# Optimization experiments

Measured on AMD Instinct MI355X. Metric: run time of the kernel, lower is better.

The kernel has to match this reference:

```python
import jax, jax.numpy as jnp
import numpy as np

N, H, E, D, L = 100000, 20000, 1600000, 64, 3
F = 4 * D  # ffn hidden = out_dim * 4


def _ln(x, g, b, eps=1e-5):
    mu = x.mean(-1, keepdims=True)
    var = ((x - mu) ** 2).mean(-1, keepdims=True)
    return (x - mu) * jax.lax.rsqrt(var + eps) * g + b


def _gconv(x, W, b, src, dst, inv_sqrt_src, inv_sqrt_dst, n_dst):
    # DGL GraphConv, norm='both': D_dst^{-1/2} A D_src^{-1/2} (x W) + b
    h = (x * inv_sqrt_src[:, None]) @ W
    agg = jax.ops.segment_sum(h[src], dst, num_segments=n_dst)
    return agg * inv_sqrt_dst[:, None] + b


def setup_inputs() -> dict:
    key = jax.random.key(0)
    ks = jax.random.split(key, 24)
    s = 0.05
    inp = {
        'node_features': jax.random.normal(ks[0], (N, D), jnp.float32),
        'edge_src': jax.random.randint(ks[1], (E,), 0, N),
        'edge_dst': jax.random.randint(ks[2], (E,), 0, H),
        'n_hyper': H,
        # stacked per-layer params [L, ...]
        'Wn2h': jax.random.normal(ks[3], (L, D, D), jnp.float32) * s,
        'bn2h': jnp.zeros((L, D), jnp.float32),
        'Wh2n': jax.random.normal(ks[4], (L, D, D), jnp.float32) * s,
        'bh2n': jnp.zeros((L, D), jnp.float32),
        'W1': jax.random.normal(ks[5], (L, D, F), jnp.float32) * s,
        'b1': jnp.zeros((L, F), jnp.float32),
        'W2': jax.random.normal(ks[6], (L, F, D), jnp.float32) * s,
        'b2': jnp.zeros((L, D), jnp.float32),
        'g1': jnp.ones((L, D), jnp.float32),
        'be1': jnp.zeros((L, D), jnp.float32),
        'g2': jnp.ones((L, D), jnp.float32),
        'be2': jnp.zeros((L, D), jnp.float32),
        'gF': jnp.ones((D,), jnp.float32),
        'bF': jnp.zeros((D,), jnp.float32),
        'Wo': jax.random.normal(ks[7], (D, D), jnp.float32) * s,
        'bo': jnp.zeros((D,), jnp.float32),
    }
    return inp


def reference(node_features, edge_src, edge_dst, n_hyper, Wn2h, bn2h, Wh2n, bh2n,
              W1, b1, W2, b2, g1, be1, g2, be2, gF, bF, Wo, bo):
    n_nodes = node_features.shape[0]
    ones = jnp.ones(edge_src.shape[0], node_features.dtype)
    deg_node = jnp.clip(jax.ops.segment_sum(ones, edge_src, num_segments=n_nodes), 1.0)
    deg_hyp = jnp.clip(jax.ops.segment_sum(ones, edge_dst, num_segments=n_hyper), 1.0)
    is_node = jax.lax.rsqrt(deg_node)  # node out-degree^{-1/2}
    is_hyp = jax.lax.rsqrt(deg_hyp)    # hyperedge in-degree^{-1/2}

    def step(h, p):
        Wa, ba, Wb, bb, w1, c1, w2, c2, gg1, ee1, gg2, ee2 = p
        # node -> hyperedge conv (unused attention output is overwritten in the original)
        h_hyper = _gconv(h, Wa, ba, edge_src, edge_dst, is_node, is_hyp, n_hyper)
        # hyperedge -> node conv on reversed graph (degrees swap roles)
        h_node = _gconv(h_hyper, Wb, bb, edge_dst, edge_src, is_hyp, is_node, n_nodes)
        h = _ln(h + h_node, gg1, ee1)
        h_ffn = jax.nn.relu(h @ w1 + c1) @ w2 + c2
        h = _ln(h + h_ffn, gg2, ee2)
        return h, None

    h, _ = jax.lax.scan(step, node_features,
                        (Wn2h, bn2h, Wh2n, bh2n, W1, b1, W2, b2, g1, be1, g2, be2))
    h = _ln(h, gF, bF)
    return h @ Wo + bo
```

## Files before the change

### kernel.cpp

```cpp
#include <hip/hip_runtime.h>

#define HYP 20000
#define NLAYER 3
#define NB_H 313
#define NB_N 391
#define PT 4096

typedef __attribute__((ext_vector_type(8))) short short8;
typedef __attribute__((ext_vector_type(4))) float floatx4;

static __device__ __forceinline__ unsigned short f2bf(float f){
  union { float f; unsigned u; } v; v.f = f;
  unsigned r = v.u + 0x7FFF + ((v.u >> 16) & 1);
  return (unsigned short)(r >> 16);
}

__global__ __launch_bounds__(256) void k_hist(const int* __restrict__ src,
    const int* __restrict__ dst, int E, int* __restrict__ bh, int* __restrict__ bn){
  __shared__ int lh[NB_H + NB_N];
  int tid = threadIdx.x;
  for (int i = tid; i < NB_H + NB_N; i += 256) lh[i] = 0;
  __syncthreads();
  for (int i = blockIdx.x*256 + tid; i < E; i += gridDim.x*256){
    atomicAdd(&lh[dst[i] >> 6], 1);
    atomicAdd(&lh[NB_H + (src[i] >> 8)], 1);
  }
  __syncthreads();
  for (int i = tid; i < NB_H; i += 256) if (lh[i]) atomicAdd(&bh[i], lh[i]);
  for (int i = tid; i < NB_N; i += 256) if (lh[NB_H+i]) atomicAdd(&bn[i], lh[NB_H+i]);
}

__global__ __launch_bounds__(256) void k_bscan(const int* __restrict__ bh,
    const int* __restrict__ bn, int* __restrict__ bstart_h, int* __restrict__ gcur_h,
    int* __restrict__ bstart_n, int* __restrict__ gcur_n){
  __shared__ int ssc[4];
  __shared__ int scarry;
  int tid = threadIdx.x, lane = tid & 63, wv = tid >> 6;
  if (tid == 0) scarry = 0;
  __syncthreads();
  for (int base = 0; base < NB_H; base += 256){
    int i = base + tid; int v = (i < NB_H) ? bh[i] : 0; int x = v;
    #pragma unroll
    for (int o = 1; o < 64; o <<= 1){ int t = __shfl_up(x,o,64); if (lane >= o) x += t; }
    if (lane == 63) ssc[wv] = x;
    __syncthreads();
    int add = (wv>0?ssc[0]:0)+(wv>1?ssc[1]:0)+(wv>2?ssc[2]:0);
    int c = scarry;
    if (i < NB_H){ int ex = c + add + x - v; bstart_h[i] = ex; gcur_h[i] = ex; }
    __syncthreads();
    if (tid == 255) scarry = c + ssc[0]+ssc[1]+ssc[2]+ssc[3];
    __syncthreads();
  }
  if (tid == 0){ bstart_h[NB_H] = scarry; scarry = 0; }
  __syncthreads();
  for (int base = 0; base < NB_N; base += 256){
    int i = base + tid; int v = (i < NB_N) ? bn[i] : 0; int x = v;
    #pragma unroll
    for (int o = 1; o < 64; o <<= 1){ int t = __shfl_up(x,o,64); if (lane >= o) x += t; }
    if (lane == 63) ssc[wv] = x;
    __syncthreads();
    int add = (wv>0?ssc[0]:0)+(wv>1?ssc[1]:0)+(wv>2?ssc[2]:0);
    int c = scarry;
    if (i < NB_N){ int ex = c + add + x - v; bstart_n[i] = ex; gcur_n[i] = ex; }
    __syncthreads();
    if (tid == 255) scarry = c + ssc[0]+ssc[1]+ssc[2]+ssc[3];
    __syncthreads();
  }
  if (tid == 0) bstart_n[NB_N] = scarry;
}

__global__ __launch_bounds__(256) void k_partition(const int* __restrict__ keys,
    const int* __restrict__ pays, int E, int keyshift, int nb,
    int* __restrict__ gcur, unsigned* __restrict__ Ebuf){
  __shared__ unsigned sst[PT];
  __shared__ int lh[NB_N], lpre[NB_N], gb[NB_N];
  __shared__ int ssc[4];
  __shared__ int scarry;
  int tid = threadIdx.x, lane = tid & 63, wv = tid >> 6;
  int base = blockIdx.x*PT;
  int m = min(PT, E - base);
  for (int i = tid; i < nb; i += 256) lh[i] = 0;
  if (tid == 0) scarry = 0;
  __syncthreads();
  unsigned en[16]; int rk[16];
  #pragma unroll
  for (int j = 0; j < 16; ++j){
    int i = base + j*256 + tid;
    if (i < E){
      unsigned k = (unsigned)keys[i], p = (unsigned)pays[i];
      en[j] = (k << keyshift) | p;
      rk[j] = atomicAdd(&lh[en[j] >> 23], 1);
    } else { en[j] = 0; rk[j] = -1; }
  }
  __syncthreads();
  for (int b2 = 0; b2 < nb; b2 += 256){
    int i = b2 + tid; int v = (i < nb) ? lh[i] : 0; int x = v;
    #pragma unroll
    for (int o = 1; o < 64; o <<= 1){ int t = __shfl_up(x,o,64); if (lane >= o) x += t; }
    if (lane == 63) ssc[wv] = x;
    __syncthreads();
    int add = (wv>0?ssc[0]:0)+(wv>1?ssc[1]:0)+(wv>2?ssc[2]:0);
    int c = scarry;
    if (i < nb) lpre[i] = c + add + x - v;
    __syncthreads();
    if (tid == 255) scarry = c + ssc[0]+ssc[1]+ssc[2]+ssc[3];
    __syncthreads();
  }
  for (int i = tid; i < nb; i += 256) gb[i] = atomicAdd(&gcur[i], lh[i]);
  #pragma unroll
  for (int j = 0; j < 16; ++j){
    if (rk[j] >= 0){
      int bk = en[j] >> 23;
      sst[lpre[bk] + rk[j]] = en[j];
    }
  }
  __syncthreads();
  for (int j = tid; j < m; j += 256){
    unsigned e = sst[j];
    int bk = e >> 23;
    Ebuf[gb[bk] + (j - lpre[bk])] = e;
  }
}

__global__ __launch_bounds__(256) void k_build(const unsigned* __restrict__ Ebuf,
    const int* __restrict__ bstart, int keyshift, int ipb, int paymask, int limit,
    int* __restrict__ off, float* __restrict__ isv, int* __restrict__ csr){
  __shared__ int lcnt[256], lpre2[256], lcur[256];
  int tid = threadIdx.x, lane = tid & 63, wv = tid >> 6;
  int b = blockIdx.x;
  int base = bstart[b], m = bstart[b+1] - base;
  for (int i = tid; i < ipb; i += 256) lcnt[i] = 0;
  __syncthreads();
  for (int i = tid; i < m; i += 256){
    unsigned e = Ebuf[base + i];
    atomicAdd(&lcnt[(e >> keyshift) & (ipb-1)], 1);
  }
  __syncthreads();
  if (wv == 0){
    int carry = 0;
    for (int c = 0; c < ipb; c += 64){
      int li = c + lane;
      int v = lcnt[li]; int x = v;
      #pragma unroll
      for (int o = 1; o < 64; o <<= 1){ int t = __shfl_up(x,o,64); if (lane >= o) x += t; }
      int ex = carry + x - v;
      int id = b*ipb + li;
      if (id <= limit) off[id] = base + ex;
      if (id < limit) isv[id] = rsqrtf((float)(v > 0 ? v : 1));
      lpre2[li] = ex;
      carry += __shfl(x, 63, 64);
    }
  }
  for (int i = tid; i < ipb; i += 256) lcur[i] = 0;
  __syncthreads();
  for (int i = tid; i < m; i += 256){
    unsigned e = Ebuf[base + i];
    int li = (e >> keyshift) & (ipb-1);
    int pos = base + lpre2[li] + atomicAdd(&lcur[li], 1);
    csr[pos] = (int)(e & (unsigned)paymask);
  }
}

__global__ void k_prescale(const float* __restrict__ x, const float* __restrict__ isn,
                           unsigned short* __restrict__ xb, int nrows){
  int i = blockIdx.x*blockDim.x + threadIdx.x;
  int st = gridDim.x*blockDim.x;
  int tot = nrows*64;
  for (; i < tot; i += st){ xb[i] = f2bf(x[i]*isn[i >> 6]); }
}

__global__ void k_cvtall(const float* __restrict__ W1, const float* __restrict__ W2,
                         const float* __restrict__ Wa, const float* __restrict__ Wb,
                         const float* __restrict__ Wo,
                         unsigned short* __restrict__ W1T, unsigned short* __restrict__ W2T,
                         unsigned short* __restrict__ WaT, unsigned short* __restrict__ WbT,
                         unsigned short* __restrict__ WoT){
  int st = gridDim.x*blockDim.x;
  int t0 = blockIdx.x*blockDim.x + threadIdx.x;
  for (int j = t0; j < NLAYER*16384; j += st){
    int l = j >> 14, n = (j >> 6) & 255, k = j & 63;
    W1T[j] = f2bf(W1[l*16384 + k*256 + n]);
  }
  for (int j = t0; j < NLAYER*16384; j += st){
    int l = j >> 14, o = (j >> 8) & 63, kk = j & 255;
    W2T[j] = f2bf(W2[l*16384 + kk*64 + o]);
  }
  for (int j = t0; j < NLAYER*4096; j += st){
    int l = j >> 12, n = (j >> 6) & 63, k = j & 63;
    WaT[j] = f2bf(Wa[l*4096 + k*64 + n]);
  }
  for (int j = t0; j < NLAYER*4096; j += st){
    int l = j >> 12, n = (j >> 6) & 63, k = j & 63;
    WbT[j] = f2bf(Wb[l*4096 + k*64 + n]);
  }
  for (int j = t0; j < 4096; j += st){
    int n = (j >> 6) & 63, k = j & 63;
    WoT[j] = f2bf(Wo[k*64 + n]);
  }
}

template<int LSTR>
static __device__ __forceinline__ void stage64(const unsigned short* __restrict__ gsrc,
    unsigned short* __restrict__ ldst, int tid, int rows){
  int nch = rows*8;
  for (int idx = tid; idx < nch; idx += 256){
    int row = idx >> 3, kc = (idx & 7)*8;
    uint4 v = *(const uint4*)&gsrc[row*64 + kc];
    *(uint4*)&ldst[row*LSTR + kc] = v;
  }
}

#define ACC8(u) \
  a0 += __uint_as_float(u.x << 16); a1 += __uint_as_float(u.x & 0xFFFF0000u); \
  a2 += __uint_as_float(u.y << 16); a3 += __uint_as_float(u.y & 0xFFFF0000u); \
  a4 += __uint_as_float(u.z << 16); a5 += __uint_as_float(u.z & 0xFFFF0000u); \
  a6 += __uint_as_float(u.w << 16); a7 += __uint_as_float(u.w & 0xFFFF0000u);

__global__ __launch_bounds__(256) void k_gather8(const unsigned short* __restrict__ feat,
    const int* __restrict__ csr, const int* __restrict__ off,
    unsigned short* __restrict__ agg, int nrows){
  int lane = threadIdx.x & 63, wvi = threadIdx.x >> 6;
  int g = lane >> 3;
  int ch = (lane & 7) * 8;
  int r = blockIdx.x*4 + wvi, stride = gridDim.x*4;
  for (; r < nrows; r += stride){
    int b = off[r], e = off[r+1];
    float a0=0,a1=0,a2=0,a3=0,a4=0,a5=0,a6=0,a7=0;
    int t = b;
    for (; t + 32 <= e; t += 32){
      int s0 = csr[t + g];
      int s1 = csr[t + 8 + g];
      int s2 = csr[t + 16 + g];
      int s3 = csr[t + 24 + g];
      uint4 u0 = *(const uint4*)&feat[(size_t)s0*64 + ch];
      uint4 u1 = *(const uint4*)&feat[(size_t)s1*64 + ch];
      uint4 u2 = *(const uint4*)&feat[(size_t)s2*64 + ch];
      uint4 u3 = *(const uint4*)&feat[(size_t)s3*64 + ch];
      ACC8(u0); ACC8(u1); ACC8(u2); ACC8(u3);
    }
    for (; t + 16 <= e; t += 16){
      int s0 = csr[t + g];
      int s1 = csr[t + 8 + g];
      uint4 u0 = *(const uint4*)&feat[(size_t)s0*64 + ch];
      uint4 u1 = *(const uint4*)&feat[(size_t)s1*64 + ch];
      ACC8(u0); ACC8(u1);
    }
    for (; t < e; t += 8){
      int idx = t + g;
      bool valid = idx < e;
      int s = csr[valid ? idx : b];
      uint4 u = *(const uint4*)&feat[(size_t)s*64 + ch];
      if (!valid){ u.x = 0; u.y = 0; u.z = 0; u.w = 0; }
      ACC8(u);
    }
    #pragma unroll
    for (int o = 8; o <= 32; o <<= 1){
      a0 += __shfl_xor(a0,o,64); a1 += __shfl_xor(a1,o,64);
      a2 += __shfl_xor(a2,o,64); a3 += __shfl_xor(a3,o,64);
      a4 += __shfl_xor(a4,o,64); a5 += __shfl_xor(a5,o,64);
      a6 += __shfl_xor(a6,o,64); a7 += __shfl_xor(a7,o,64);
    }
    if (g == 0){
      uint4 w;
      w.x = (unsigned)f2bf(a0) | ((unsigned)f2bf(a1) << 16);
      w.y = (unsigned)f2bf(a2) | ((unsigned)f2bf(a3) << 16);
      w.z = (unsigned)f2bf(a4) | ((unsigned)f2bf(a5) << 16);
      w.w = (unsigned)f2bf(a6) | ((unsigned)f2bf(a7) << 16);
      *(uint4*)&agg[(size_t)r*64 + ch] = w;
    }
  }
}

__global__ __launch_bounds__(256) void k_mmA(const unsigned short* __restrict__ aggb,
    const unsigned short* __restrict__ WaT, const float* __restrict__ bias,
    const float* __restrict__ ihy, unsigned short* __restrict__ ouths, int nrows){
  __shared__ unsigned short sWb[64*72];
  int tid = threadIdx.x;
  int lane = tid & 63, w = tid >> 6;
  int quad = lane >> 4, n16 = lane & 15;
  stage64<72>(WaT, sWb, tid, 64);
  __syncthreads();
  int rowbase = blockIdx.x*64 + w*16;
  int arow = min(rowbase + n16, nrows-1);
  short8 a0 = *(const short8*)&aggb[(size_t)arow*64 + quad*8];
  short8 a1 = *(const short8*)&aggb[(size_t)arow*64 + 32 + quad*8];
  float ih[4];
  #pragma unroll
  for (int r = 0; r < 4; ++r) ih[r] = ihy[min(rowbase + quad*4 + r, nrows-1)];
  #pragma unroll
  for (int ot = 0; ot < 4; ++ot){
    floatx4 c = (floatx4){0.f,0.f,0.f,0.f};
    short8 b0 = *(const short8*)&sWb[(ot*16+n16)*72 + quad*8];
    short8 b1 = *(const short8*)&sWb[(ot*16+n16)*72 + 32 + quad*8];
    c = __builtin_amdgcn_mfma_f32_16x16x32_bf16(a0, b0, c, 0, 0, 0);
    c = __builtin_amdgcn_mfma_f32_16x16x32_bf16(a1, b1, c, 0, 0, 0);
    float bl = bias[ot*16 + n16];
    #pragma unroll
    for (int r = 0; r < 4; ++r){
      int rr = rowbase + quad*4 + r;
      if (rr < nrows)
        ouths[(size_t)rr*64 + ot*16 + n16] = f2bf(fmaf(c[r], ih[r], bl) * ih[r]);
    }
  }
}

__global__ __launch_bounds__(256) void k_fused(
    const unsigned short* __restrict__ aggb,
    const unsigned short* __restrict__ WbT,
    const float* __restrict__ bbg,
    const float* __restrict__ isn,
    const float* __restrict__ hin,
    const float* __restrict__ g1v, const float* __restrict__ be1v,
    const unsigned short* __restrict__ W1T, const float* __restrict__ b1g,
    const unsigned short* __restrict__ W2T, const float* __restrict__ b2g,
    const float* __restrict__ g2v, const float* __restrict__ be2v,
    float* __restrict__ Outp, unsigned short* __restrict__ Qs, int nrows)
{
  __shared__ unsigned short sW1T[128*72];
  __shared__ unsigned short sW2T[64*136];
  __shared__ unsigned short sPH[4*16*72];
  unsigned short* sWb = sW1T;
  int tid = threadIdx.x;
  int lane = tid & 63, w = tid >> 6;
  int quad = lane >> 4, n16 = lane & 15;
  int rb[2];
  rb[0] = blockIdx.x*128 + w*16;
  rb[1] = rb[0] + 64;

  stage64<72>(WbT, sWb, tid, 64);
  __syncthreads();

  float pP[2][4][4];
  float isr[2][4];
  #pragma unroll
  for (int s = 0; s < 2; ++s){
    int arow = min(rb[s] + n16, nrows-1);
    short8 a0 = *(const short8*)&aggb[(size_t)arow*64 + quad*8];
    short8 a1 = *(const short8*)&aggb[(size_t)arow*64 + 32 + quad*8];
    #pragma unroll
    for (int r = 0; r < 4; ++r) isr[s][r] = isn[min(rb[s] + quad*4 + r, nrows-1)];
    #pragma unroll
    for (int ot = 0; ot < 4; ++ot){
      floatx4 c = (floatx4){0.f,0.f,0.f,0.f};
      short8 b0 = *(const short8*)&sWb[(ot*16+n16)*72 + quad*8];
      short8 b1 = *(const short8*)&sWb[(ot*16+n16)*72 + 32 + quad*8];
      c = __builtin_amdgcn_mfma_f32_16x16x32_bf16(a0, b0, c, 0, 0, 0);
      c = __builtin_amdgcn_mfma_f32_16x16x32_bf16(a1, b1, c, 0, 0, 0);
      float bb = bbg[ot*16 + n16];
      #pragma unroll
      for (int r = 0; r < 4; ++r){
        int rr = min(rb[s] + quad*4 + r, nrows-1);
        pP[s][ot][r] = fmaf(c[r], isr[s][r], bb) + hin[(size_t)rr*64 + ot*16 + n16];
      }
    }
  }
  {
    float gl[4], bl[4];
    #pragma unroll
    for (int ot = 0; ot < 4; ++ot){ gl[ot] = g1v[ot*16+n16]; bl[ot] = be1v[ot*16+n16]; }
    #pragma unroll
    for (int s = 0; s < 2; ++s)
      #pragma unroll
      for (int r = 0; r < 4; ++r){
        float sv = (pP[s][0][r] + pP[s][1][r]) + (pP[s][2][r] + pP[s][3][r]);
        float q = fmaf(pP[s][0][r], pP[s][0][r], pP[s][1][r]*pP[s][1][r]) +
                  fmaf(pP[s][2][r], pP[s][2][r], pP[s][3][r]*pP[s][3][r]);
        #pragma unroll
        for (int o = 8; o >= 1; o >>= 1){
          sv += __shfl_xor(sv, o, 64);
          q  += __shfl_xor(q, o, 64);
        }
        float mu = sv*(1.f/64.f);
        float var = fmaf(-mu, mu, q*(1.f/64.f));
        float rs = rsqrtf(var + 1e-5f);
        #pragma unroll
        for (int ot = 0; ot < 4; ++ot)
          pP[s][ot][r] = fmaf((pP[s][ot][r]-mu)*rs, gl[ot], bl[ot]);
      }
  }
  unsigned short* myP = &sPH[w*16*72];
  short8 p0[2], p1[2];
  #pragma unroll
  for (int s = 0; s < 2; ++s){
    #pragma unroll
    for (int ot = 0; ot < 4; ++ot)
      #pragma unroll
      for (int r = 0; r < 4; ++r)
        myP[(quad*4 + r)*72 + ot*16 + n16] = f2bf(pP[s][ot][r]);
    p0[s] = *(const short8*)&myP[n16*72 + quad*8];
    p1[s] = *(const short8*)&myP[n16*72 + 32 + quad*8];
  }

  floatx4 acc2[2][4];
  #pragma unroll
  for (int s = 0; s < 2; ++s)
    #pragma unroll
    for (int t = 0; t < 4; ++t) acc2[s][t] = (floatx4){0.f,0.f,0.f,0.f};
  unsigned short* myHc = &sPH[w*16*72];

  for (int hb = 0; hb < 2; ++hb){
    __syncthreads();
    stage64<72>(W1T + hb*128*64, sW1T, tid, 128);
    for (int idx = tid; idx < 1024; idx += 256){
      int o = idx >> 4, kc = (idx & 15)*8;
      uint4 v = *(const uint4*)&W2T[o*256 + hb*128 + kc];
      *(uint4*)&sW2T[o*136 + kc] = v;
    }
    __syncthreads();

    for (int ck = 0; ck < 4; ++ck){
      #pragma unroll
      for (int s = 0; s < 2; ++s){
        #pragma unroll
        for (int nt = 0; nt < 2; ++nt){
          int nn = ck*32 + nt*16 + n16;
          floatx4 c = (floatx4){0.f,0.f,0.f,0.f};
          short8 b0 = *(const short8*)&sW1T[nn*72 + quad*8];
          short8 b1f = *(const short8*)&sW1T[nn*72 + 32 + quad*8];
          c = __builtin_amdgcn_mfma_f32_16x16x32_bf16(p0[s], b0, c, 0, 0, 0);
          c = __builtin_amdgcn_mfma_f32_16x16x32_bf16(p1[s], b1f, c, 0, 0, 0);
          float bb = b1g[hb*128 + nn];
          #pragma unroll
          for (int r = 0; r < 4; ++r){
            float h = fmaxf(c[r] + bb, 0.f);
            myHc[(quad*4 + r)*40 + nt*16 + n16] = f2bf(h);
          }
        }
        short8 a2 = *(const short8*)&myHc[n16*40 + quad*8];
        #pragma unroll
        for (int ot = 0; ot < 4; ++ot){
          short8 b2f = *(const short8*)&sW2T[(ot*16 + n16)*136 + ck*32 + quad*8];
          acc2[s][ot] = __builtin_amdgcn_mfma_f32_16x16x32_bf16(a2, b2f, acc2[s][ot], 0, 0, 0);
        }
      }
    }
  }

  float gl[4], bel[4];
  #pragma unroll
  for (int ot = 0; ot < 4; ++ot){ gl[ot] = g2v[ot*16 + n16]; bel[ot] = be2v[ot*16 + n16]; }
  #pragma unroll
  for (int s = 0; s < 2; ++s){
    float pre[4][4];
    #pragma unroll
    for (int ot = 0; ot < 4; ++ot){
      float b2c = b2g[ot*16 + n16];
      #pragma unroll
      for (int r = 0; r < 4; ++r)
        pre[ot][r] = acc2[s][ot][r] + b2c + pP[s][ot][r];
    }
    #pragma unroll
    for (int r = 0; r < 4; ++r){
      float sv = (pre[0][r] + pre[1][r]) + (pre[2][r] + pre[3][r]);
      float q = fmaf(pre[0][r], pre[0][r], pre[1][r]*pre[1][r]) +
                fmaf(pre[2][r], pre[2][r], pre[3][r]*pre[3][r]);
      #pragma unroll
      for (int o = 8; o >= 1; o >>= 1){
        sv += __shfl_xor(sv, o, 64);
        q  += __shfl_xor(q, o, 64);
      }
      float mu = sv*(1.f/64.f);
      float var = fmaf(-mu, mu, q*(1.f/64.f));
      float rs = rsqrtf(var + 1e-5f);
      int rr = rb[s] + quad*4 + r;
      if (rr < nrows){
        float isr2 = isn[rr];
        #pragma unroll
        for (int ot = 0; ot < 4; ++ot){
          float ov = fmaf((pre[ot][r]-mu)*rs, gl[ot], bel[ot]);
          Outp[(size_t)rr*64 + ot*16 + n16] = ov;
          Qs[(size_t)rr*64 + ot*16 + n16] = f2bf(ov * isr2);
        }
      }
    }
  }
}

__global__ __launch_bounds__(256) void k_final(const float* __restrict__ Q,
    const unsigned short* __restrict__ WoT, const float* __restrict__ bog,
    const float* __restrict__ gF, const float* __restrict__ bF,
    float* __restrict__ out, int nrows){
  __shared__ unsigned short sWb[64*72];
  int tid = threadIdx.x;
  int lane = tid & 63, w = tid >> 6;
  int quad = lane >> 4, n16 = lane & 15;
  stage64<72>(WoT, sWb, tid, 64);
  __syncthreads();
  int rowbase = blockIdx.x*64 + w*16;
  int arow = min(rowbase + n16, nrows-1);
  float4 q0 = *(const float4*)&Q[(size_t)arow*64 + quad*8];
  float4 q1 = *(const float4*)&Q[(size_t)arow*64 + quad*8 + 4];
  float4 q2 = *(const float4*)&Q[(size_t)arow*64 + 32 + quad*8];
  float4 q3 = *(const float4*)&Q[(size_t)arow*64 + 32 + quad*8 + 4];
  float s = (q0.x+q0.y+q0.z+q0.w) + (q1.x+q1.y+q1.z+q1.w)
          + (q2.x+q2.y+q2.z+q2.w) + (q3.x+q3.y+q3.z+q3.w);
  float qq = (q0.x*q0.x+q0.y*q0.y+q0.z*q0.z+q0.w*q0.w)
           + (q1.x*q1.x+q1.y*q1.y+q1.z*q1.z+q1.w*q1.w)
           + (q2.x*q2.x+q2.y*q2.y+q2.z*q2.z+q2.w*q2.w)
           + (q3.x*q3.x+q3.y*q3.y+q3.z*q3.z+q3.w*q3.w);
  s += __shfl_xor(s, 16, 64);  qq += __shfl_xor(qq, 16, 64);
  s += __shfl_xor(s, 32, 64);  qq += __shfl_xor(qq, 32, 64);
  float mu = s*(1.f/64.f);
  float var = fmaf(-mu, mu, qq*(1.f/64.f));
  float rs = rsqrtf(var + 1e-5f);
  float4 g0 = *(const float4*)&gF[quad*8];
  float4 g1 = *(const float4*)&gF[quad*8 + 4];
  float4 g2 = *(const float4*)&gF[32 + quad*8];
  float4 g3 = *(const float4*)&gF[32 + quad*8 + 4];
  float4 f0 = *(const float4*)&bF[quad*8];
  float4 f1 = *(const float4*)&bF[quad*8 + 4];
  float4 f2 = *(const float4*)&bF[32 + quad*8];
  float4 f3 = *(const float4*)&bF[32 + quad*8 + 4];
  short8 a0, a1;
  a0[0]=f2bf(fmaf((q0.x-mu)*rs, g0.x, f0.x)); a0[1]=f2bf(fmaf((q0.y-mu)*rs, g0.y, f0.y));
  a0[2]=f2bf(fmaf((q0.z-mu)*rs, g0.z, f0.z)); a0[3]=f2bf(fmaf((q0.w-mu)*rs, g0.w, f0.w));
  a0[4]=f2bf(fmaf((q1.x-mu)*rs, g1.x, f1.x)); a0[5]=f2bf(fmaf((q1.y-mu)*rs, g1.y, f1.y));
  a0[6]=f2bf(fmaf((q1.z-mu)*rs, g1.z, f1.z)); a0[7]=f2bf(fmaf((q1.w-mu)*rs, g1.w, f1.w));
  a1[0]=f2bf(fmaf((q2.x-mu)*rs, g2.x, f2.x)); a1[1]=f2bf(fmaf((q2.y-mu)*rs, g2.y, f2.y));
  a1[2]=f2bf(fmaf((q2.z-mu)*rs, g2.z, f2.z)); a1[3]=f2bf(fmaf((q2.w-mu)*rs, g2.w, f2.w));
  a1[4]=f2bf(fmaf((q3.x-mu)*rs, g3.x, f3.x)); a1[5]=f2bf(fmaf((q3.y-mu)*rs, g3.y, f3.y));
  a1[6]=f2bf(fmaf((q3.z-mu)*rs, g3.z, f3.z)); a1[7]=f2bf(fmaf((q3.w-mu)*rs, g3.w, f3.w));
  #pragma unroll
  for (int ot = 0; ot < 4; ++ot){
    floatx4 c = (floatx4){0.f,0.f,0.f,0.f};
    short8 b0 = *(const short8*)&sWb[(ot*16+n16)*72 + quad*8];
    short8 b1 = *(const short8*)&sWb[(ot*16+n16)*72 + 32 + quad*8];
    c = __builtin_amdgcn_mfma_f32_16x16x32_bf16(a0, b0, c, 0, 0, 0);
    c = __builtin_amdgcn_mfma_f32_16x16x32_bf16(a1, b1, c, 0, 0, 0);
    float bol = bog[ot*16 + n16];
    #pragma unroll
    for (int r = 0; r < 4; ++r){
      int rr = rowbase + quad*4 + r;
      if (rr < nrows) out[(size_t)rr*64 + ot*16 + n16] = c[r] + bol;
    }
  }
}

extern "C" void kernel_launch(void* const* d_in, const int* in_sizes, int n_in,
                              void* d_out, int out_size, void* d_ws, size_t ws_size,
                              hipStream_t stream){
  const float* nf   = (const float*)d_in[0];
  const int*   esrc = (const int*)d_in[1];
  const int*   edst = (const int*)d_in[2];
  const float* Wn2h = (const float*)d_in[4];
  const float* bn2h = (const float*)d_in[5];
  const float* Wh2n = (const float*)d_in[6];
  const float* bh2n = (const float*)d_in[7];
  const float* W1   = (const float*)d_in[8];
  const float* b1   = (const float*)d_in[9];
  const float* W2   = (const float*)d_in[10];
  const float* b2   = (const float*)d_in[11];
  const float* g1   = (const float*)d_in[12];
  const float* be1  = (const float*)d_in[13];
  const float* g2   = (const float*)d_in[14];
  const float* be2  = (const float*)d_in[15];
  const float* gF   = (const float*)d_in[16];
  const float* bF   = (const float*)d_in[17];
  const float* Wo   = (const float*)d_in[18];
  const float* bo   = (const float*)d_in[19];
  const int N = in_sizes[0] / 64;
  const int E = in_sizes[1];
  const int H = HYP;
  float* out = (float*)d_out;

  char* w = (char*)d_ws;
  auto carve = [&](size_t bytes) -> char* {
    char* p = w; w += (bytes + 255) & ~(size_t)255; return p;
  };
  int* bh = (int*)carve((size_t)(NB_H + NB_N)*4);
  int* bn = bh + NB_H;
  int* bstart_h = (int*)carve((size_t)(NB_H+1)*4);
  int* gcur_h   = (int*)carve((size_t)NB_H*4);
  int* bstart_n = (int*)carve((size_t)(NB_N+1)*4);
  int* gcur_n   = (int*)carve((size_t)NB_N*4);
  unsigned* Ebuf_h = (unsigned*)carve((size_t)E*4);
  unsigned* Ebuf_n = (unsigned*)carve((size_t)E*4);
  int*   off_h = (int*)carve((size_t)(H+1)*4);
  int*   off_n = (int*)carve((size_t)(N+1)*4);
  float* is_h  = (float*)carve((size_t)H*4);
  float* is_n  = (float*)carve((size_t)N*4);
  int*   csr_h = (int*)carve((size_t)E*4);
  int*   csr_n = (int*)carve((size_t)E*4);
  unsigned short* aggxb = (unsigned short*)carve((size_t)H*64*2);
  unsigned short* agghb = (unsigned short*)carve((size_t)N*64*2);
  float* Qb    = (float*)carve((size_t)N*64*4);
  unsigned short* hhsb = (unsigned short*)carve((size_t)H*64*2);
  unsigned short* xb0  = (unsigned short*)carve((size_t)N*64*2);
  unsigned short* Qs   = (unsigned short*)carve((size_t)N*64*2);
  unsigned short* W1g16 = (unsigned short*)carve((size_t)NLAYER*64*256*2);
  unsigned short* W2g16 = (unsigned short*)carve((size_t)NLAYER*256*64*2);
  unsigned short* Wag16 = (unsigned short*)carve((size_t)NLAYER*4096*2);
  unsigned short* Wbg16 = (unsigned short*)carve((size_t)NLAYER*4096*2);
  unsigned short* Wog16 = (unsigned short*)carve((size_t)4096*2);

  hipMemsetAsync(bh, 0, (size_t)(NB_H + NB_N)*4, stream);
  k_cvtall<<<96, 256, 0, stream>>>(W1, W2, Wn2h, Wh2n, Wo,
                                   W1g16, W2g16, Wag16, Wbg16, Wog16);
  k_hist<<<512, 256, 0, stream>>>(esrc, edst, E, bh, bn);
  k_bscan<<<1, 256, 0, stream>>>(bh, bn, bstart_h, gcur_h, bstart_n, gcur_n);
  k_partition<<<(E + PT - 1)/PT, 256, 0, stream>>>(edst, esrc, E, 17, NB_H, gcur_h, Ebuf_h);
  k_partition<<<(E + PT - 1)/PT, 256, 0, stream>>>(esrc, edst, E, 15, NB_N, gcur_n, Ebuf_n);
  k_build<<<NB_H, 256, 0, stream>>>(Ebuf_h, bstart_h, 17, 64, 0x1FFFF, H, off_h, is_h, csr_h);
  k_build<<<NB_N, 256, 0, stream>>>(Ebuf_n, bstart_n, 15, 256, 0x7FFF, N, off_n, is_n, csr_n);
  k_prescale<<<4096, 256, 0, stream>>>(nf, is_n, xb0, N);

  const int NB64 = (N + 63)/64;
  const int NB128 = (N + 127)/128;
  const int HB64 = (H + 63)/64;
  for (int l = 0; l < NLAYER; ++l){
    const float* hin = (l == 0) ? nf : Qb;
    const unsigned short* hsrc = (l == 0) ? xb0 : Qs;
    k_gather8<<<2048, 256, 0, stream>>>(hsrc, csr_h, off_h, aggxb, H);
    k_mmA<<<HB64, 256, 0, stream>>>(aggxb, Wag16 + l*4096, bn2h + l*64, is_h, hhsb, H);
    k_gather8<<<2048, 256, 0, stream>>>(hhsb, csr_n, off_n, agghb, N);
    k_fused<<<NB128, 256, 0, stream>>>(agghb, Wbg16 + l*4096, bh2n + l*64, is_n, hin,
                                       g1 + l*64, be1 + l*64,
                                       W1g16 + l*64*256, b1 + l*256,
                                       W2g16 + l*256*64, b2 + l*64,
                                       g2 + l*64, be2 + l*64, Qb, Qs, N);
  }
  k_final<<<NB64, 256, 0, stream>>>(Qb, Wog16, bo, gF, bF, out, N);
}
```

Baseline: 537.5 us.

## Restructure fused FFN kernel to 64-row blocks with swizzled LDS weight tiles

The fused node-side kernel now processes 64 rows per block instead of 128, stages W1/W2 in four 64-wide chunks into XOR-swizzled unpadded LDS tiles, and sets an occupancy hint of 6 blocks per SM. This lowers LDS and register use per block so more blocks can be resident and avoids bank conflicts, at the cost of re-staging weights for twice as many blocks and more barriers. The hyperedge matmul kernel moves to 64-thread blocks of 16 rows, and prescale is vectorised to 8 elements per thread.

```diff
diff --git a/kernel.cpp b/kernel.cpp
--- a/kernel.cpp
+++ b/kernel.cpp
@@ -165,8 +165,18 @@
                            unsigned short* __restrict__ xb, int nrows){
   int i = blockIdx.x*blockDim.x + threadIdx.x;
   int st = gridDim.x*blockDim.x;
-  int tot = nrows*64;
-  for (; i < tot; i += st){ xb[i] = f2bf(x[i]*isn[i >> 6]); }
+  int tot = nrows*8;
+  for (; i < tot; i += st){
+    float s = isn[i >> 3];
+    float4 v0 = *(const float4*)&x[(size_t)i*8];
+    float4 v1 = *(const float4*)&x[(size_t)i*8 + 4];
+    uint4 o;
+    o.x = (unsigned)f2bf(v0.x*s) | ((unsigned)f2bf(v0.y*s) << 16);
+    o.y = (unsigned)f2bf(v0.z*s) | ((unsigned)f2bf(v0.w*s) << 16);
+    o.z = (unsigned)f2bf(v1.x*s) | ((unsigned)f2bf(v1.y*s) << 16);
+    o.w = (unsigned)f2bf(v1.z*s) | ((unsigned)f2bf(v1.w*s) << 16);
+    *(uint4*)&xb[(size_t)i*8] = o;
+  }
 }
 
 __global__ void k_cvtall(const float* __restrict__ W1, const float* __restrict__ W2,
@@ -208,6 +218,22 @@
     uint4 v = *(const uint4*)&gsrc[row*64 + kc];
     *(uint4*)&ldst[row*LSTR + kc] = v;
   }
+}
+
+static __device__ __forceinline__ void stage_swz(const unsigned short* __restrict__ g,
+    int gs, unsigned short* __restrict__ l, int tid){
+  #pragma unroll
+  for (int it = 0; it < 2; ++it){
+    int c = it*256 + tid;
+    int row = c >> 3, s = c & 7;
+    uint4 v = *(const uint4*)&g[row*gs + s*8];
+    *(uint4*)&l[(row << 6) + ((((unsigned)(s ^ row)) & 7u) << 3)] = v;
+  }
+}
+
+static __device__ __forceinline__ short8 rdswz(const unsigned short* __restrict__ l,
+    int row, int slot){
+  return *(const short8*)&l[(row << 6) + ((((unsigned)(slot ^ row)) & 7u) << 3)];
 }
 
 #define ACC8(u) \
@@ -271,16 +297,18 @@
   }
 }
 
-__global__ __launch_bounds__(256) void k_mmA(const unsigned short* __restrict__ aggb,
+__global__ __launch_bounds__(64) void k_mmA(const unsigned short* __restrict__ aggb,
     const unsigned short* __restrict__ WaT, const float* __restrict__ bias,
     const float* __restrict__ ihy, unsigned short* __restrict__ ouths, int nrows){
   __shared__ unsigned short sWb[64*72];
-  int tid = threadIdx.x;
-  int lane = tid & 63, w = tid >> 6;
+  int lane = threadIdx.x;
   int quad = lane >> 4, n16 = lane & 15;
-  stage64<72>(WaT, sWb, tid, 64);
-  __syncthreads();
-  int rowbase = blockIdx.x*64 + w*16;
+  for (int idx = lane; idx < 512; idx += 64){
+    int row = idx >> 3, kc = (idx & 7)*8;
+    *(uint4*)&sWb[row*72 + kc] = *(const uint4*)&WaT[row*64 + kc];
+  }
+  __syncthreads();
+  int rowbase = blockIdx.x*16;
   int arow = min(rowbase + n16, nrows-1);
   short8 a0 = *(const short8*)&aggb[(size_t)arow*64 + quad*8];
   short8 a1 = *(const short8*)&aggb[(size_t)arow*64 + 32 + quad*8];
@@ -304,7 +332,7 @@
   }
 }
 
-__global__ __launch_bounds__(256) void k_fused(
+__global__ __launch_bounds__(256, 6) void k_fused(
     const unsigned short* __restrict__ aggb,
     const unsigned short* __restrict__ WbT,
     const float* __restrict__ bbg,
@@ -316,41 +344,37 @@
     const float* __restrict__ g2v, const float* __restrict__ be2v,
     float* __restrict__ Outp, unsigned short* __restrict__ Qs, int nrows)
 {
-  __shared__ unsigned short sW1T[128*72];
-  __shared__ unsigned short sW2T[64*136];
+  __shared__ unsigned short sA[64*64];
+  __shared__ unsigned short sB[64*64];
   __shared__ unsigned short sPH[4*16*72];
-  unsigned short* sWb = sW1T;
   int tid = threadIdx.x;
   int lane = tid & 63, w = tid >> 6;
   int quad = lane >> 4, n16 = lane & 15;
-  int rb[2];
-  rb[0] = blockIdx.x*128 + w*16;
-  rb[1] = rb[0] + 64;
-
-  stage64<72>(WbT, sWb, tid, 64);
-  __syncthreads();
-
-  float pP[2][4][4];
-  float isr[2][4];
-  #pragma unroll
-  for (int s = 0; s < 2; ++s){
-    int arow = min(rb[s] + n16, nrows-1);
+  int rb = blockIdx.x*64 + w*16;
+
+  stage_swz(WbT, 64, sA, tid);
+  __syncthreads();
+
+  float pP[4][4];
+  float isr[4];
+  {
+    int arow = min(rb + n16, nrows-1);
     short8 a0 = *(const short8*)&aggb[(size_t)arow*64 + quad*8];
     short8 a1 = *(const short8*)&aggb[(size_t)arow*64 + 32 + quad*8];
     #pragma unroll
-    for (int r = 0; r < 4; ++r) isr[s][r] = isn[min(rb[s] + quad*4 + r, nrows-1)];
+    for (int r = 0; r < 4; ++r) isr[r] = isn[min(rb + quad*4 + r, nrows-1)];
     #pragma unroll
     for (int ot = 0; ot < 4; ++ot){
       floatx4 c = (floatx4){0.f,0.f,0.f,0.f};
-      short8 b0 = *(const short8*)&sWb[(ot*16+n16)*72 + quad*8];
-      short8 b1 = *(const short8*)&sWb[(ot*16+n16)*72 + 32 + quad*8];
+      short8 b0 = rdswz(sA, ot*16+n16, quad);
+      short8 b1 = rdswz(sA, ot*16+n16, 4+quad);
       c = __builtin_amdgcn_mfma_f32_16x16x32_bf16(a0, b0, c, 0, 0, 0);
       c = __builtin_amdgcn_mfma_f32_16x16x32_bf16(a1, b1, c, 0, 0, 0);
       float bb = bbg[ot*16 + n16];
       #pragma unroll
       for (int r = 0; r < 4; ++r){
-        int rr = min(rb[s] + quad*4 + r, nrows-1);
-        pP[s][ot][r] = fmaf(c[r], isr[s][r], bb) + hin[(size_t)rr*64 + ot*16 + n16];
+        int rr = min(rb + quad*4 + r, nrows-1);
+        pP[ot][r] = fmaf(c[r], isr[r], bb) + hin[(size_t)rr*64 + ot*16 + n16];
       }
     }
   }
@@ -359,101 +383,10 @@
     #pragma unroll
     for (int ot = 0; ot < 4; ++ot){ gl[ot] = g1v[ot*16+n16]; bl[ot] = be1v[ot*16+n16]; }
     #pragma unroll
-    for (int s = 0; s < 2; ++s)
-      #pragma unroll
-      for (int r = 0; r < 4; ++r){
-        float sv = (pP[s][0][r] + pP[s][1][r]) + (pP[s][2][r] + pP[s][3][r]);
-        float q = fmaf(pP[s][0][r], pP[s][0][r], pP[s][1][r]*pP[s][1][r]) +
-                  fmaf(pP[s][2][r], pP[s][2][r], pP[s][3][r]*pP[s][3][r]);
-        #pragma unroll
-        for (int o = 8; o >= 1; o >>= 1){
-          sv += __shfl_xor(sv, o, 64);
-          q  += __shfl_xor(q, o, 64);
-        }
-        float mu = sv*(1.f/64.f);
-        float var = fmaf(-mu, mu, q*(1.f/64.f));
-        float rs = rsqrtf(var + 1e-5f);
-        #pragma unroll
-        for (int ot = 0; ot < 4; ++ot)
-          pP[s][ot][r] = fmaf((pP[s][ot][r]-mu)*rs, gl[ot], bl[ot]);
-      }
-  }
-  unsigned short* myP = &sPH[w*16*72];
-  short8 p0[2], p1[2];
-  #pragma unroll
-  for (int s = 0; s < 2; ++s){
-    #pragma unroll
-    for (int ot = 0; ot < 4; ++ot)
-      #pragma unroll
-      for (int r = 0; r < 4; ++r)
-        myP[(quad*4 + r)*72 + ot*16 + n16] = f2bf(pP[s][ot][r]);
-    p0[s] = *(const short8*)&myP[n16*72 + quad*8];
-    p1[s] = *(const short8*)&myP[n16*72 + 32 + quad*8];
-  }
-
-  floatx4 acc2[2][4];
-  #pragma unroll
-  for (int s = 0; s < 2; ++s)
-    #pragma unroll
-    for (int t = 0; t < 4; ++t) acc2[s][t] = (floatx4){0.f,0.f,0.f,0.f};
-  unsigned short* myHc = &sPH[w*16*72];
-
-  for (int hb = 0; hb < 2; ++hb){
-    __syncthreads();
-    stage64<72>(W1T + hb*128*64, sW1T, tid, 128);
-    for (int idx = tid; idx < 1024; idx += 256){
-      int o = idx >> 4, kc = (idx & 15)*8;
-      uint4 v = *(const uint4*)&W2T[o*256 + hb*128 + kc];
-      *(uint4*)&sW2T[o*136 + kc] = v;
-    }
-    __syncthreads();
-
-    for (int ck = 0; ck < 4; ++ck){
-      #pragma unroll
-      for (int s = 0; s < 2; ++s){
-        #pragma unroll
-        for (int nt = 0; nt < 2; ++nt){
-          int nn = ck*32 + nt*16 + n16;
-          floatx4 c = (floatx4){0.f,0.f,0.f,0.f};
-          short8 b0 = *(const short8*)&sW1T[nn*72 + quad*8];
-          short8 b1f = *(const short8*)&sW1T[nn*72 + 32 + quad*8];
-          c = __builtin_amdgcn_mfma_f32_16x16x32_bf16(p0[s], b0, c, 0, 0, 0);
-          c = __builtin_amdgcn_mfma_f32_16x16x32_bf16(p1[s], b1f, c, 0, 0, 0);
-          float bb = b1g[hb*128 + nn];
-          #pragma unroll
-          for (int r = 0; r < 4; ++r){
-            float h = fmaxf(c[r] + bb, 0.f);
-            myHc[(quad*4 + r)*40 + nt*16 + n16] = f2bf(h);
-          }
-        }
-        short8 a2 = *(const short8*)&myHc[n16*40 + quad*8];
-        #pragma unroll
-        for (int ot = 0; ot < 4; ++ot){
-          short8 b2f = *(const short8*)&sW2T[(ot*16 + n16)*136 + ck*32 + quad*8];
-          acc2[s][ot] = __builtin_amdgcn_mfma_f32_16x16x32_bf16(a2, b2f, acc2[s][ot], 0, 0, 0);
-        }
-      }
-    }
-  }
-
-  float gl[4], bel[4];
-  #pragma unroll
-  for (int ot = 0; ot < 4; ++ot){ gl[ot] = g2v[ot*16 + n16]; bel[ot] = be2v[ot*16 + n16]; }
-  #pragma unroll
-  for (int s = 0; s < 2; ++s){
-    float pre[4][4];
-    #pragma unroll
-    for (int ot = 0; ot < 4; ++ot){
-      float b2c = b2g[ot*16 + n16];
-      #pragma unroll
-      for (int r = 0; r < 4; ++r)
-        pre[ot][r] = acc2[s][ot][r] + b2c + pP[s][ot][r];
-    }
-    #pragma unroll
     for (int r = 0; r < 4; ++r){
-      float sv = (pre[0][r] + pre[1][r]) + (pre[2][r] + pre[3][r]);
-      float q = fmaf(pre[0][r], pre[0][r], pre[1][r]*pre[1][r]) +
-                fmaf(pre[2][r], pre[2][r], pre[3][r]*pre[3][r]);
+      float sv = (pP[0][r] + pP[1][r]) + (pP[2][r] + pP[3][r]);
+      float q = fmaf(pP[0][r], pP[0][r], pP[1][r]*pP[1][r]) +
+                fmaf(pP[2][r], pP[2][r], pP[3][r]*pP[3][r]);
       #pragma unroll
       for (int o = 8; o >= 1; o >>= 1){
         sv += __shfl_xor(sv, o, 64);
@@ -462,7 +395,83 @@
       float mu = sv*(1.f/64.f);
       float var = fmaf(-mu, mu, q*(1.f/64.f));
       float rs = rsqrtf(var + 1e-5f);
-      int rr = rb[s] + quad*4 + r;
+      #pragma unroll
+      for (int ot = 0; ot < 4; ++ot)
+        pP[ot][r] = fmaf((pP[ot][r]-mu)*rs, gl[ot], bl[ot]);
+    }
+  }
+  unsigned short* myP = &sPH[w*16*72];
+  #pragma unroll
+  for (int ot = 0; ot < 4; ++ot)
+    #pragma unroll
+    for (int r = 0; r < 4; ++r)
+      myP[(quad*4 + r)*72 + ot*16 + n16] = f2bf(pP[ot][r]);
+  short8 p0 = *(const short8*)&myP[n16*72 + quad*8];
+  short8 p1 = *(const short8*)&myP[n16*72 + 32 + quad*8];
+
+  floatx4 acc2[4];
+  #pragma unroll
+  for (int t = 0; t < 4; ++t) acc2[t] = (floatx4){0.f,0.f,0.f,0.f};
+  unsigned short* myHc = myP;
+
+  for (int q = 0; q < 4; ++q){
+    __syncthreads();
+    stage_swz(W1T + q*64*64, 64, sA, tid);
+    stage_swz(W2T + q*64, 256, sB, tid);
+    __syncthreads();
+
+    #pragma unroll
+    for (int ck2 = 0; ck2 < 2; ++ck2){
+      #pragma unroll
+      for (int nt = 0; nt < 2; ++nt){
+        int nl = ck2*32 + nt*16 + n16;
+        floatx4 c = (floatx4){0.f,0.f,0.f,0.f};
+        short8 b0 = rdswz(sA, nl, quad);
+        short8 b1f = rdswz(sA, nl, 4+quad);
+        c = __builtin_amdgcn_mfma_f32_16x16x32_bf16(p0, b0, c, 0, 0, 0);
+        c = __builtin_amdgcn_mfma_f32_16x16x32_bf16(p1, b1f, c, 0, 0, 0);
+        float bb = b1g[q*64 + nl];
+        #pragma unroll
+        for (int r = 0; r < 4; ++r){
+          float h = fmaxf(c[r] + bb, 0.f);
+          myHc[(quad*4 + r)*40 + nt*16 + n16] = f2bf(h);
+        }
+      }
+      short8 a2 = *(const short8*)&myHc[n16*40 + quad*8];
+      #pragma unroll
+      for (int ot = 0; ot < 4; ++ot){
+        short8 b2f = rdswz(sB, ot*16+n16, ck2*4 + quad);
+        acc2[ot] = __builtin_amdgcn_mfma_f32_16x16x32_bf16(a2, b2f, acc2[ot], 0, 0, 0);
+      }
+    }
+  }
+
+  {
+    float gl[4], bel[4];
+    #pragma unroll
+    for (int ot = 0; ot < 4; ++ot){ gl[ot] = g2v[ot*16 + n16]; bel[ot] = be2v[ot*16 + n16]; }
+    float pre[4][4];
+    #pragma unroll
+    for (int ot = 0; ot < 4; ++ot){
+      float b2c = b2g[ot*16 + n16];
+      #pragma unroll
+      for (int r = 0; r < 4; ++r)
+        pre[ot][r] = acc2[ot][r] + b2c + pP[ot][r];
+    }
+    #pragma unroll
+    for (int r = 0; r < 4; ++r){
+      float sv = (pre[0][r] + pre[1][r]) + (pre[2][r] + pre[3][r]);
+      float q = fmaf(pre[0][r], pre[0][r], pre[1][r]*pre[1][r]) +
+                fmaf(pre[2][r], pre[2][r], pre[3][r]*pre[3][r]);
+      #pragma unroll
+      for (int o = 8; o >= 1; o >>= 1){
+        sv += __shfl_xor(sv, o, 64);
+        q  += __shfl_xor(q, o, 64);
+      }
+      float mu = sv*(1.f/64.f);
+      float var = fmaf(-mu, mu, q*(1.f/64.f));
+      float rs = rsqrtf(var + 1e-5f);
+      int rr = rb + quad*4 + r;
       if (rr < nrows){
         float isr2 = isn[rr];
         #pragma unroll
@@ -602,22 +611,21 @@
   k_partition<<<(E + PT - 1)/PT, 256, 0, stream>>>(esrc, edst, E, 15, NB_N, gcur_n, Ebuf_n);
   k_build<<<NB_H, 256, 0, stream>>>(Ebuf_h, bstart_h, 17, 64, 0x1FFFF, H, off_h, is_h, csr_h);
   k_build<<<NB_N, 256, 0, stream>>>(Ebuf_n, bstart_n, 15, 256, 0x7FFF, N, off_n, is_n, csr_n);
-  k_prescale<<<4096, 256, 0, stream>>>(nf, is_n, xb0, N);
+  k_prescale<<<2048, 256, 0, stream>>>(nf, is_n, xb0, N);
 
   const int NB64 = (N + 63)/64;
-  const int NB128 = (N + 127)/128;
-  const int HB64 = (H + 63)/64;
+  const int HB16 = (H + 15)/16;
   for (int l = 0; l < NLAYER; ++l){
     const float* hin = (l == 0) ? nf : Qb;
     const unsigned short* hsrc = (l == 0) ? xb0 : Qs;
     k_gather8<<<2048, 256, 0, stream>>>(hsrc, csr_h, off_h, aggxb, H);
-    k_mmA<<<HB64, 256, 0, stream>>>(aggxb, Wag16 + l*4096, bn2h + l*64, is_h, hhsb, H);
+    k_mmA<<<HB16, 64, 0, stream>>>(aggxb, Wag16 + l*4096, bn2h + l*64, is_h, hhsb, H);
     k_gather8<<<2048, 256, 0, stream>>>(hhsb, csr_n, off_n, agghb, N);
-    k_fused<<<NB128, 256, 0, stream>>>(agghb, Wbg16 + l*4096, bh2n + l*64, is_n, hin,
-                                       g1 + l*64, be1 + l*64,
-                                       W1g16 + l*64*256, b1 + l*256,
-                                       W2g16 + l*256*64, b2 + l*64,
-                                       g2 + l*64, be2 + l*64, Qb, Qs, N);
+    k_fused<<<NB64, 256, 0, stream>>>(agghb, Wbg16 + l*4096, bh2n + l*64, is_n, hin,
+                                      g1 + l*64, be1 + l*64,
+                                      W1g16 + l*64*256, b1 + l*256,
+                                      W2g16 + l*256*64, b2 + l*64,
+                                      g2 + l*64, be2 + l*64, Qb, Qs, N);
   }
   k_final<<<NB64, 256, 0, stream>>>(Qb, Wog16, bo, gF, bF, out, N);
 }
```

Result: no change. 534.9 us (-0.5%).
